# Kernel optimization log

Hardware: AMD Instinct MI355X
Metric: run time of the kernel (lower is better)

Reference implementation:

```python
import jax, jax.numpy as jnp
import numpy as np

B = 2048
N_USERS = 100000
N_ITEMS = 50000
N = N_USERS + N_ITEMS
EMB = 64
NNZ = 100000


def setup_inputs() -> dict:
    key = jax.random.key(0)
    k1, k2, k3, k4 = jax.random.split(key, 4)
    u_id = jax.random.randint(k1, (B,), 0, N_USERS, dtype=jnp.int64 if jax.config.jax_enable_x64 else jnp.int32)
    pos_i_id = jax.random.randint(k2, (B,), 0, N, dtype=u_id.dtype)
    train_mask = jax.random.randint(k3, (2, NNZ), 0, B, dtype=u_id.dtype)
    all_embed = jax.random.normal(k4, (N, EMB), dtype=jnp.float32)
    return {"u_id": u_id, "pos_i_id": pos_i_id, "train_mask": train_mask, "all_embed": all_embed}


def reference(u_id, pos_i_id, train_mask, all_embed):
    # policy_type == 'uij': scores = (u_e + pos_e) @ all_e^T  -> [B, N]
    u_e = all_embed[u_id]
    pos_e = all_embed[pos_i_id]
    scores = jnp.einsum("bd,nd->bn", u_e + pos_e, all_embed)
    # Note: the original computes a sparse train-mask tensor (sp_mask) but never
    # uses it; only the zero->-inf masking below affects the output.
    logits = jnp.where(scores == 0.0, -jnp.inf, scores)
    probs = jax.nn.softmax(logits, axis=1)  # [B, N]
    # Categorical sampling per row (fixed key for reproducibility)
    samples = jax.random.categorical(jax.random.key(42), logits, axis=1)  # [B]
    selected_neg_prob = jnp.take_along_axis(probs, samples[:, None], axis=1)[:, 0]
    return samples, selected_neg_prob
```

## Files before the change

### kernel.cpp

```cpp
#include <hip/hip_runtime.h>
#include <stdint.h>

#define B_ROWS   2048
#define N_COLS   150000
#define NSTRIPS  128
#define CHUNK    128
#define NCHUNK   1172
#define ROWG     16

#define NEG_HUGE (-3.0e38f)
#define G_SPAN_HARD  20.6f
#define G_MAX_MARGIN 15.944f
#define EPS_B        2.0e-4f
#define G_FILTER_SLACK 1e-5f

#define WS_MPART 0
#define WS_ZPART (B_ROWS * NSTRIPS)
#define WS_CMAX  (2 * B_ROWS * NSTRIPS)
#define WS_M     (WS_CMAX + B_ROWS * NCHUNK)
#define WS_Z     (WS_M + B_ROWS)
#define WS_VLB   (WS_Z + B_ROWS)
#define WS_CSTAR (WS_VLB + B_ROWS)
#define WS_BEST  (WS_CSTAR + B_ROWS)
#define WS_ENORM (WS_BEST + 2 * B_ROWS)
#define WS_QNORM (WS_ENORM + 2048)
#define WS_EHI   (WS_QNORM + B_ROWS)
#define WS_ELO   (WS_EHI + NCHUNK * 4096)
#define WS_END   (WS_ELO + NCHUNK * 4096)

typedef __attribute__((ext_vector_type(8))) unsigned short ushort8;
typedef __attribute__((ext_vector_type(8))) short short8;
typedef __attribute__((ext_vector_type(4))) float f32x4;

__device__ __forceinline__ uint32_t rotl32(uint32_t x, int r) {
  return (x << r) | (x >> (32 - r));
}

__device__ __forceinline__ void threefry2x32_k42(uint32_t& x0, uint32_t& x1) {
  const uint32_t ks0 = 0u;
  const uint32_t ks1 = 42u;
  const uint32_t ks2 = 0x1BD11BDAu ^ 0u ^ 42u;
  x0 += ks0; x1 += ks1;
#define TF_R(r) { x0 += x1; x1 = rotl32(x1, (r)); x1 ^= x0; }
  TF_R(13) TF_R(15) TF_R(26) TF_R(6)
  x0 += ks1; x1 += ks2 + 1u;
  TF_R(17) TF_R(29) TF_R(16) TF_R(24)
  x0 += ks2; x1 += ks0 + 2u;
  TF_R(13) TF_R(15) TF_R(26) TF_R(6)
  x0 += ks0; x1 += ks1 + 3u;
  TF_R(17) TF_R(29) TF_R(16) TF_R(24)
  x0 += ks1; x1 += ks2 + 4u;
  TF_R(13) TF_R(15) TF_R(26) TF_R(6)
  x0 += ks2; x1 += ks0 + 5u;
#undef TF_R
}

__device__ __forceinline__ float gumbel_from_bits(uint32_t bits) {
  const uint32_t mant = bits >> 9;
  const float f = __uint_as_float(mant | 0x3f800000u) - 1.0f;
  const float l1 = mant ? log1pf(f - 1.0f) : -87.33654475055311f;
  return -__logf(-l1);
}

__device__ __forceinline__ float gumbel_at(uint32_t flat_idx) {
  uint32_t x0 = 0u, x1 = flat_idx;
  threefry2x32_k42(x0, x1);
  return gumbel_from_bits(x0 ^ x1);
}

__device__ __forceinline__ unsigned long long pack_vn(float v, int n) {
  uint32_t u = __float_as_uint(v);
  u ^= ((uint32_t)((int32_t)u >> 31)) | 0x80000000u;
  return ((unsigned long long)u << 32) | (uint32_t)(0xFFFFFFFFu - (uint32_t)n);
}

__device__ __forceinline__ float unpack_v(unsigned long long p) {
  uint32_t u = (uint32_t)(p >> 32);
  u = (u & 0x80000000u) ? (u ^ 0x80000000u) : ~u;
  return __uint_as_float(u);
}

__device__ __forceinline__ int unpack_n(unsigned long long p) {
  return (int)(0xFFFFFFFFu - (uint32_t)(p & 0xFFFFFFFFull));
}

__device__ __forceinline__ unsigned long long umax64(unsigned long long a,
                                                     unsigned long long b) {
  return a > b ? a : b;
}

__device__ __forceinline__ float dot_q_e(const float4* q4, const float4* e4) {
  float s = 0.0f;
#pragma unroll
  for (int k4 = 0; k4 < 16; ++k4) {
    const float4 e = e4[k4];
    const float4 q = q4[k4];
    s = fmaf(q.x, e.x, s);
    s = fmaf(q.y, e.y, s);
    s = fmaf(q.z, e.z, s);
    s = fmaf(q.w, e.w, s);
  }
  return s;
}

__device__ __forceinline__ unsigned short f32_to_bf16_rne(float f) {
  const uint32_t u = __float_as_uint(f);
  return (unsigned short)((u + 0x7fffu + ((u >> 16) & 1u)) >> 16);
}
__device__ __forceinline__ float bf16_to_f32(unsigned short h) {
  return __uint_as_float(((uint32_t)h) << 16);
}

__global__ __launch_bounds__(256) void advnet_enorm(const float* __restrict__ emb,
                                                    float* __restrict__ ws) {
  const int c = blockIdx.x;
  const int t = threadIdx.x;
  const int lane = t & 63;
  const int row = t >> 1;
  const int n = c * CHUNK + row;
  float ss = 0.0f;
  if (n < N_COLS) {
    const float4* p = (const float4*)emb + (size_t)n * 16 + (t & 1) * 8;
#pragma unroll
    for (int i = 0; i < 8; ++i) {
      const float4 v = p[i];
      ss = fmaf(v.x, v.x, ss); ss = fmaf(v.y, v.y, ss);
      ss = fmaf(v.z, v.z, ss); ss = fmaf(v.w, v.w, ss);
    }
  }
  ss += __shfl_xor(ss, 1, 64);
  float mx = ss;
  for (int off = 2; off < 64; off <<= 1) mx = fmaxf(mx, __shfl_xor(mx, off, 64));
  __shared__ float sm[4];
  if (lane == 0) sm[t >> 6] = mx;
  __syncthreads();
  if (t == 0)
    ws[WS_ENORM + c] =
        sqrtf(fmaxf(fmaxf(sm[0], sm[1]), fmaxf(sm[2], sm[3]))) * 1.00002f;
}

__global__ __launch_bounds__(256) void advnet_ebuild(const float* __restrict__ emb,
                                                     float* __restrict__ ws) {
  const int c = blockIdx.x;
  const int t = threadIdx.x;
  char* hi_b = (char*)(ws + WS_EHI) + (size_t)c * 16384;
  char* lo_b = (char*)(ws + WS_ELO) + (size_t)c * 16384;
#pragma unroll
  for (int k = 0; k < 4; ++k) {
    const int j = t + 256 * k;
    const int row = j >> 3, kq = j & 7;
    const int n = c * CHUNK + row;
    ushort8 hi = (ushort8)0, lo = (ushort8)0;
    if (n < N_COLS) {
      const float4* ep = (const float4*)emb + (size_t)n * 16 + kq * 2;
      const float4 a0 = ep[0], a1 = ep[1];
      const float e[8] = {a0.x, a0.y, a0.z, a0.w, a1.x, a1.y, a1.z, a1.w};
#pragma unroll
      for (int j8 = 0; j8 < 8; ++j8) {
        const unsigned short h = f32_to_bf16_rne(e[j8]);
        hi[j8] = h;
        lo[j8] = f32_to_bf16_rne(e[j8] - bf16_to_f32(h));
      }
    }
    const int gz = kq ^ (row & 7);
    *(ushort8*)(hi_b + (size_t)(row * 8 + gz) * 16) = hi;
    *(ushort8*)(lo_b + (size_t)(row * 8 + gz) * 16) = lo;
  }
}

__device__ __forceinline__ void stage_tbl(const char* tb_hi, const char* tb_lo,
                                          unsigned short* eh, unsigned short* el,
                                          int c, int wave, int lane) {
  const size_t cb = (size_t)c * 16384 + (size_t)(wave * 1024 + lane * 16);
  const int wo = wave * 1024;
#pragma unroll
  for (int i = 0; i < 4; ++i) {
    const int off = i * 4096;
    __builtin_amdgcn_global_load_lds(
        (const __attribute__((address_space(1))) void*)(tb_hi + cb + off),
        (__attribute__((address_space(3))) void*)((char*)eh + wo + off), 16, 0, 0);
    __builtin_amdgcn_global_load_lds(
        (const __attribute__((address_space(1))) void*)(tb_lo + cb + off),
        (__attribute__((address_space(3))) void*)((char*)el + wo + off), 16, 0, 0);
  }
}

__device__ __forceinline__ void stage_conv(const float* __restrict__ emb,
                                           unsigned short* eh, unsigned short* el,
                                           int c, int tid) {
  const int n0 = c * CHUNK;
#pragma unroll
  for (int k = 0; k < 4; ++k) {
    const int p = tid + 256 * k;
    const int row = p >> 3, kq = p & 7;
    const int n = n0 + row;
    ushort8 hi = (ushort8)0, lo = (ushort8)0;
    if (n < N_COLS) {
      const float4* ep = (const float4*)emb + (size_t)n * 16 + kq * 2;
      const float4 a0 = ep[0], a1 = ep[1];
      const float e[8] = {a0.x, a0.y, a0.z, a0.w, a1.x, a1.y, a1.z, a1.w};
#pragma unroll
      for (int j = 0; j < 8; ++j) {
        const unsigned short h = f32_to_bf16_rne(e[j]);
        hi[j] = h;
        lo[j] = f32_to_bf16_rne(e[j] - bf16_to_f32(h));
      }
    }
    const int off = row * 64 + ((kq * 8) ^ ((row & 7) << 3));
    *(ushort8*)&eh[off] = hi;
    *(ushort8*)&el[off] = lo;
  }
}

template <bool TBL>
__global__ __launch_bounds__(256, 2) void advnet_gemm(
    const int* __restrict__ u_id, const int* __restrict__ pos_id,
    const float* __restrict__ emb, float* __restrict__ ws) {
  __shared__ unsigned short eh0[8192], el0[8192], eh1[8192], el1[8192];

  const int tid = threadIdx.x;
  const int bid = blockIdx.x;
  const int rg = bid / NSTRIPS;
  const int strip = bid - rg * NSTRIPS;
  const int wave = tid >> 6;
  const int lane = tid & 63;
  const int lc = lane & 15;
  const int lg = lane >> 4;

#pragma unroll
  for (int k = 0; k < 4; ++k) {
    const int p = tid + 256 * k;
    const int row = p >> 3, kq = p & 7;
    const int b = rg * 128 + row;
    const float4* ua = (const float4*)emb + (size_t)u_id[b] * 16 + kq * 2;
    const float4* pa = (const float4*)emb + (size_t)pos_id[b] * 16 + kq * 2;
    const float4 a0 = ua[0], a1 = ua[1], c0 = pa[0], c1 = pa[1];
    const float q[8] = {a0.x + c0.x, a0.y + c0.y, a0.z + c0.z, a0.w + c0.w,
                        a1.x + c1.x, a1.y + c1.y, a1.z + c1.z, a1.w + c1.w};
    ushort8 hi, lo;
#pragma unroll
    for (int j = 0; j < 8; ++j) {
      const unsigned short h = f32_to_bf16_rne(q[j]);
      hi[j] = h;
      lo[j] = f32_to_bf16_rne(q[j] - bf16_to_f32(h));
    }
    const int off = row * 64 + ((kq * 8) ^ ((row & 7) << 3));
    *(ushort8*)&eh0[off] = hi;
    *(ushort8*)&el0[off] = lo;
  }
  __syncthreads();

  short8 qh_r[2][2], ql_r[2][2];
#pragma unroll
  for (int kh = 0; kh < 2; ++kh)
#pragma unroll
    for (int rt = 0; rt < 2; ++rt) {
      const int r = wave * 32 + rt * 16 + lc;
      const int off = r * 64 + (((kh * 4 + lg) * 8) ^ ((r & 7) << 3));
      qh_r[kh][rt] = *(const short8*)&eh0[off];
      ql_r[kh][rt] = *(const short8*)&el0[off];
    }
  __syncthreads();

  float m[8], Z[8];
#pragma unroll
  for (int s = 0; s < 8; ++s) { m[s] = NEG_HUGE; Z[s] = 0.0f; }

  const char* tb_hi = (const char*)(ws + WS_EHI);
  const char* tb_lo = (const char*)(ws + WS_ELO);

  if (TBL) stage_tbl(tb_hi, tb_lo, eh0, el0, strip, wave, lane);
  else     stage_conv(emb, eh0, el0, strip, tid);
  __syncthreads();

  int cur = 0;
  for (int c = strip; c < NCHUNK; c += NSTRIPS) {
    unsigned short* EH  = cur ? eh1 : eh0;
    unsigned short* EL  = cur ? el1 : el0;
    unsigned short* EHn = cur ? eh0 : eh1;
    unsigned short* ELn = cur ? el0 : el1;
    if (c + NSTRIPS < NCHUNK) {
      if (TBL) stage_tbl(tb_hi, tb_lo, EHn, ELn, c + NSTRIPS, wave, lane);
      else     stage_conv(emb, EHn, ELn, c + NSTRIPS, tid);
    }

    f32x4 acc[2][8];
#pragma unroll
    for (int rt = 0; rt < 2; ++rt)
#pragma unroll
      for (int ct = 0; ct < 8; ++ct) acc[rt][ct] = (f32x4){0.f, 0.f, 0.f, 0.f};

#pragma unroll
    for (int kh = 0; kh < 2; ++kh) {
#pragma unroll
      for (int ct = 0; ct < 8; ++ct) {
        const int col = ct * 16 + lc;
        const int off = col * 64 + (((kh * 4 + lg) * 8) ^ ((col & 7) << 3));
        const short8 ehf = *(const short8*)&EH[off];
        const short8 elf = *(const short8*)&EL[off];
#pragma unroll
        for (int rt = 0; rt < 2; ++rt) {
          acc[rt][ct] = __builtin_amdgcn_mfma_f32_16x16x32_bf16(qh_r[kh][rt], ehf, acc[rt][ct], 0, 0, 0);
          acc[rt][ct] = __builtin_amdgcn_mfma_f32_16x16x32_bf16(qh_r[kh][rt], elf, acc[rt][ct], 0, 0, 0);
          acc[rt][ct] = __builtin_amdgcn_mfma_f32_16x16x32_bf16(ql_r[kh][rt], ehf, acc[rt][ct], 0, 0, 0);
        }
      }
    }

#pragma unroll
    for (int rt = 0; rt < 2; ++rt) {
#pragma unroll
      for (int j = 0; j < 4; ++j) {
        const int s = rt * 4 + j;
        float sp[8];
        float cm = NEG_HUGE;
#pragma unroll
        for (int ct = 0; ct < 8; ++ct) {
          const float v = acc[rt][ct][j];
          sp[ct] = (v != 0.0f) ? v : NEG_HUGE;
          cm = fmaxf(cm, sp[ct]);
        }
        const float nm = fmaxf(m[s], cm);
        float za = 0.0f;
#pragma unroll
        for (int ct = 0; ct < 8; ++ct) za += __expf(sp[ct] - nm);
        Z[s] = Z[s] * __expf(m[s] - nm) + za;
        m[s] = nm;
        float cr = cm;
        cr = fmaxf(cr, __shfl_xor(cr, 1, 64));
        cr = fmaxf(cr, __shfl_xor(cr, 2, 64));
        cr = fmaxf(cr, __shfl_xor(cr, 4, 64));
        cr = fmaxf(cr, __shfl_xor(cr, 8, 64));
        if (lc == 0) {
          const int row = rg * 128 + wave * 32 + rt * 16 + lg * 4 + j;
          ws[WS_CMAX + (size_t)row * NCHUNK + c] = cr;
        }
      }
    }
    __syncthreads();
    cur ^= 1;
  }

#pragma unroll
  for (int rt = 0; rt < 2; ++rt) {
#pragma unroll
    for (int j = 0; j < 4; ++j) {
      const int s = rt * 4 + j;
      float mi = m[s], Zi = Z[s];
      for (int off = 1; off < 16; off <<= 1) {
        const float om = __shfl_xor(mi, off, 64);
        const float oZ = __shfl_xor(Zi, off, 64);
        const float nm = fmaxf(mi, om);
        Zi = Zi * __expf(mi - nm) + oZ * __expf(om - nm);
        mi = nm;
      }
      if (lc == 0) {
        const int row = rg * 128 + wave * 32 + rt * 16 + lg * 4 + j;
        ws[WS_MPART + (size_t)row * NSTRIPS + strip] = mi;
        ws[WS_ZPART + (size_t)row * NSTRIPS + strip] = Zi;
      }
    }
  }
}

__global__ __launch_bounds__(128) void advnet_rowstat(
    const int* __restrict__ u_id, const int* __restrict__ pos_id,
    const float* __restrict__ emb, float* __restrict__ ws) {
  const int r = blockIdx.x;
  const int t = threadIdx.x;

  __shared__ float sA[2], sB[2];
  __shared__ unsigned long long sP[2];
  __shared__ float qrow[64];

  const size_t idx = (size_t)r * NSTRIPS + t;
  const float ms = ws[WS_MPART + idx];
  const float zs = ws[WS_ZPART + idx];
  float M = ms;
  for (int off = 1; off < 64; off <<= 1) M = fmaxf(M, __shfl_xor(M, off, 64));
  if ((t & 63) == 0) sA[t >> 6] = M;
  __syncthreads();
  M = fmaxf(sA[0], sA[1]);
  float z = zs * __expf(ms - M);
  for (int off = 1; off < 64; off <<= 1) z += __shfl_xor(z, off, 64);
  if ((t & 63) == 0) sB[t >> 6] = z;
  __syncthreads();
  const float Z = sB[0] + sB[1];

  unsigned long long cp = 0ull;
  for (int c = t; c < NCHUNK; c += 128)
    cp = umax64(cp, pack_vn(ws[WS_CMAX + (size_t)r * NCHUNK + c], c));
  for (int off = 1; off < 64; off <<= 1)
    cp = umax64(cp, __shfl_xor(cp, off, 64));
  if ((t & 63) == 0) sP[t >> 6] = cp;
  __syncthreads();
  cp = umax64(sP[0], sP[1]);
  const int cstar = unpack_n(cp);

  if (t < 16) {
    const float4 a = ((const float4*)emb)[(size_t)u_id[r] * 16 + t];
    const float4 c = ((const float4*)emb)[(size_t)pos_id[r] * 16 + t];
    ((float4*)qrow)[t] = make_float4(a.x + c.x, a.y + c.y, a.z + c.z, a.w + c.w);
  }
  __syncthreads();

  {
    const float qv = qrow[t & 63];
    float ss = qv * qv;
    for (int off = 1; off < 64; off <<= 1) ss += __shfl_xor(ss, off, 64);
    if (t == 0) ws[WS_QNORM + r] = sqrtf(ss) * 1.00002f;
  }

  unsigned long long bp = 0ull;
  const int n = cstar * CHUNK + t;
  if (n < N_COLS) {
    const float s = dot_q_e((const float4*)qrow, (const float4*)emb + (size_t)n * 16);
    if (s != 0.0f && s >= M - G_SPAN_HARD) {
      const uint32_t L = (uint32_t)r * (uint32_t)N_COLS + (uint32_t)n;
      bp = pack_vn(gumbel_at(L) + s, n);
    }
  }
  for (int off = 1; off < 64; off <<= 1)
    bp = umax64(bp, __shfl_xor(bp, off, 64));
  if ((t & 63) == 0) sP[t >> 6] = bp;
  __syncthreads();
  if (t == 0) {
    const unsigned long long best = umax64(sP[0], sP[1]);
    ((unsigned long long*)(ws + WS_BEST))[r] = best;
    ws[WS_VLB + r] = unpack_v(best);
    ws[WS_M + r] = M;
    ws[WS_Z + r] = Z;
    ((int*)ws)[WS_CSTAR + r] = cstar;
  }
}

#define SVCAP 2048
__global__ __launch_bounds__(256) void advnet_pick(
    const int* __restrict__ u_id, const int* __restrict__ pos_id,
    const float* __restrict__ emb, float* __restrict__ ws) {
  const int r = blockIdx.x >> 1;
  const int par = blockIdx.x & 1;
  const int t = threadIdx.x;

  __shared__ float qrow[64];
  __shared__ unsigned short cq[600];
  __shared__ float cqg[600];
  __shared__ unsigned int svpk[SVCAP];
  __shared__ float svg[SVCAP];
  __shared__ int cqn, svn;
  __shared__ unsigned long long sred[4];

  if (t == 0) { cqn = 0; svn = 0; }
  if (t < 16) {
    const float4 a = ((const float4*)emb)[(size_t)u_id[r] * 16 + t];
    const float4 c = ((const float4*)emb)[(size_t)pos_id[r] * 16 + t];
    ((float4*)qrow)[t] = make_float4(a.x + c.x, a.y + c.y, a.z + c.z, a.w + c.w);
  }
  const float vlb = ws[WS_VLB + r];
  const float bq = ws[WS_QNORM + r] * EPS_B;
  const int cstar = ((const int*)ws)[WS_CSTAR + r];
  __syncthreads();

  for (int c = par + 2 * t; c < NCHUNK; c += 512) {
    if (c == cstar) continue;
    const float cm = ws[WS_CMAX + (size_t)r * NCHUNK + c];
    const float gth = vlb - cm - bq * ws[WS_ENORM + c];
    if (gth < G_MAX_MARGIN) {
      const int k = atomicAdd(&cqn, 1);
      cq[k] = (unsigned short)c;
      cqg[k] = gth;
    }
  }
  __syncthreads();
  const int nq = cqn;
  const float4* qr4 = (const float4*)qrow;

  unsigned long long bp = 0ull;

  for (int base = 0; base < nq; base += 8) {
    if (svn > SVCAP - 1024) {
      __syncthreads();
      const int cnt = svn;
      for (int k = t; k < cnt; k += 256) {
        const int n = (int)svpk[k];
        const float s = dot_q_e(qr4, (const float4*)emb + (size_t)n * 16);
        if (s != 0.0f) bp = umax64(bp, pack_vn(svg[k] + s, n));
      }
      __syncthreads();
      if (t == 0) svn = 0;
      __syncthreads();
    }
#pragma unroll
    for (int u = 0; u < 4; ++u) {
      const int idx = t + 256 * u;
      const int slot = base + (idx >> 7);
      if (slot < nq) {
        const int n = (int)cq[slot] * CHUNK + (idx & 127);
        if (n < N_COLS) {
          const float g = gumbel_at((uint32_t)r * (uint32_t)N_COLS + (uint32_t)n);
          if (g > cqg[slot] - G_FILTER_SLACK) {
            const int k = atomicAdd(&svn, 1);
            if (k < SVCAP) { svpk[k] = (unsigned)n; svg[k] = g; }
          }
        }
      }
    }
    __syncthreads();
  }

  {
    const int cnt = svn < SVCAP ? svn : SVCAP;
    for (int k = t; k < cnt; k += 256) {
      const int n = (int)svpk[k];
      const float s = dot_q_e(qr4, (const float4*)emb + (size_t)n * 16);
      if (s != 0.0f) bp = umax64(bp, pack_vn(svg[k] + s, n));
    }
  }

  for (int off = 1; off < 64; off <<= 1)
    bp = umax64(bp, __shfl_xor(bp, off, 64));
  if ((t & 63) == 0) sred[t >> 6] = bp;
  __syncthreads();
  if (t == 0) {
    const unsigned long long b =
        umax64(umax64(sred[0], sred[1]), umax64(sred[2], sred[3]));
    if (b) atomicMax((unsigned long long*)(ws + WS_BEST) + r, b);
  }
}

__global__ __launch_bounds__(64) void advnet_final(
    const int* __restrict__ u_id, const int* __restrict__ pos_id,
    const float* __restrict__ emb, const float* __restrict__ ws,
    float* __restrict__ out) {
  const int r = blockIdx.x * 64 + threadIdx.x;
  if (r >= B_ROWS) return;
  const unsigned long long w = ((const unsigned long long*)(ws + WS_BEST))[r];
  const int n = unpack_n(w);
  const float4* qa = (const float4*)emb + (size_t)u_id[r] * 16;
  const float4* qb = (const float4*)emb + (size_t)pos_id[r] * 16;
  const float4* e4 = (const float4*)emb + (size_t)n * 16;
  float s = 0.0f;
#pragma unroll
  for (int k4 = 0; k4 < 16; ++k4) {
    const float4 a = qa[k4], b = qb[k4], e = e4[k4];
    float4 q;
    q.x = a.x + b.x; q.y = a.y + b.y; q.z = a.z + b.z; q.w = a.w + b.w;
    s = fmaf(q.x, e.x, s);
    s = fmaf(q.y, e.y, s);
    s = fmaf(q.z, e.z, s);
    s = fmaf(q.w, e.w, s);
  }
  out[r] = (float)n;
  out[B_ROWS + r] = __expf(s - ws[WS_M + r]) / ws[WS_Z + r];
}

extern "C" void kernel_launch(void* const* d_in, const int* in_sizes, int n_in,
                              void* d_out, int out_size, void* d_ws, size_t ws_size,
                              hipStream_t stream) {
  const int* u_id = (const int*)d_in[0];
  const int* pos_id = (const int*)d_in[1];
  const float* emb = (const float*)d_in[3];
  float* ws = (float*)d_ws;
  float* out = (float*)d_out;

  const size_t need = (size_t)WS_END * 4;
  const bool tbl = ws_size >= need;

  advnet_enorm<<<dim3(NCHUNK), dim3(256), 0, stream>>>(emb, ws);
  if (tbl) {
    advnet_ebuild<<<dim3(NCHUNK), dim3(256), 0, stream>>>(emb, ws);
    advnet_gemm<true><<<dim3(ROWG * NSTRIPS), dim3(256), 0, stream>>>(
        u_id, pos_id, emb, ws);
  } else {
    advnet_gemm<false><<<dim3(ROWG * NSTRIPS), dim3(256), 0, stream>>>(
        u_id, pos_id, emb, ws);
  }
  advnet_rowstat<<<dim3(B_ROWS), dim3(128), 0, stream>>>(u_id, pos_id, emb, ws);
  advnet_pick<<<dim3(B_ROWS * 2), dim3(256), 0, stream>>>(u_id, pos_id, emb, ws);
  advnet_final<<<dim3(B_ROWS / 64), dim3(64), 0, stream>>>(u_id, pos_id, emb, ws, out);
}
```

Before: 306.9 us.

## Fold enorm into ebuild, single-buffer GEMM LDS, use exp2 with pre-scaled queries

The row-norm computation moves into the ebuild kernel, so one launch and one full read of the embedding table go away when the workspace is large enough. The GEMM drops LDS double buffering for a single buffer, which raises the occupancy hint from 2 to 5 blocks per CU but serialises loads and compute inside each block. Queries are pre-scaled by log2(e) so the online softmax can use the native exp2. The explicit zero-score masking in the max/sum loop is removed, and the sampling filter slack is loosened to absorb the extra rounding.

```diff
diff --git a/kernel.cpp b/kernel.cpp
--- a/kernel.cpp
+++ b/kernel.cpp
@@ -12,7 +12,16 @@
 #define G_SPAN_HARD  20.6f
 #define G_MAX_MARGIN 15.944f
 #define EPS_B        2.0e-4f
-#define G_FILTER_SLACK 1e-5f
+#define G_FILTER_SLACK 3e-5f
+
+#define LOG2E_F 1.44269504088896340736f
+#define LN2_F   0.69314718055994530942f
+
+#if __has_builtin(__builtin_amdgcn_exp2f)
+#define EXP2F(x) __builtin_amdgcn_exp2f(x)
+#else
+#define EXP2F(x) exp2f(x)
+#endif
 
 #define WS_MPART 0
 #define WS_ZPART (B_ROWS * NSTRIPS)
@@ -145,12 +154,14 @@
   const int t = threadIdx.x;
   char* hi_b = (char*)(ws + WS_EHI) + (size_t)c * 16384;
   char* lo_b = (char*)(ws + WS_ELO) + (size_t)c * 16384;
+  float mx = 0.0f;
 #pragma unroll
   for (int k = 0; k < 4; ++k) {
     const int j = t + 256 * k;
     const int row = j >> 3, kq = j & 7;
     const int n = c * CHUNK + row;
     ushort8 hi = (ushort8)0, lo = (ushort8)0;
+    float ss = 0.0f;
     if (n < N_COLS) {
       const float4* ep = (const float4*)emb + (size_t)n * 16 + kq * 2;
       const float4 a0 = ep[0], a1 = ep[1];
@@ -160,12 +171,24 @@
         const unsigned short h = f32_to_bf16_rne(e[j8]);
         hi[j8] = h;
         lo[j8] = f32_to_bf16_rne(e[j8] - bf16_to_f32(h));
+        ss = fmaf(e[j8], e[j8], ss);
       }
     }
     const int gz = kq ^ (row & 7);
     *(ushort8*)(hi_b + (size_t)(row * 8 + gz) * 16) = hi;
     *(ushort8*)(lo_b + (size_t)(row * 8 + gz) * 16) = lo;
-  }
+    ss += __shfl_xor(ss, 1, 64);
+    ss += __shfl_xor(ss, 2, 64);
+    ss += __shfl_xor(ss, 4, 64);
+    mx = fmaxf(mx, ss);
+  }
+  for (int off = 8; off < 64; off <<= 1) mx = fmaxf(mx, __shfl_xor(mx, off, 64));
+  __shared__ float sm[4];
+  if ((t & 63) == 0) sm[t >> 6] = mx;
+  __syncthreads();
+  if (t == 0)
+    ws[WS_ENORM + c] =
+        sqrtf(fmaxf(fmaxf(sm[0], sm[1]), fmaxf(sm[2], sm[3]))) * 1.00002f;
 }
 
 __device__ __forceinline__ void stage_tbl(const char* tb_hi, const char* tb_lo,
@@ -213,10 +236,10 @@
 }
 
 template <bool TBL>
-__global__ __launch_bounds__(256, 2) void advnet_gemm(
+__global__ __launch_bounds__(256, 5) void advnet_gemm(
     const int* __restrict__ u_id, const int* __restrict__ pos_id,
     const float* __restrict__ emb, float* __restrict__ ws) {
-  __shared__ unsigned short eh0[8192], el0[8192], eh1[8192], el1[8192];
+  __shared__ unsigned short eh_s[8192], el_s[8192];
 
   const int tid = threadIdx.x;
   const int bid = blockIdx.x;
@@ -235,8 +258,10 @@
     const float4* ua = (const float4*)emb + (size_t)u_id[b] * 16 + kq * 2;
     const float4* pa = (const float4*)emb + (size_t)pos_id[b] * 16 + kq * 2;
     const float4 a0 = ua[0], a1 = ua[1], c0 = pa[0], c1 = pa[1];
-    const float q[8] = {a0.x + c0.x, a0.y + c0.y, a0.z + c0.z, a0.w + c0.w,
-                        a1.x + c1.x, a1.y + c1.y, a1.z + c1.z, a1.w + c1.w};
+    const float q[8] = {(a0.x + c0.x) * LOG2E_F, (a0.y + c0.y) * LOG2E_F,
+                        (a0.z + c0.z) * LOG2E_F, (a0.w + c0.w) * LOG2E_F,
+                        (a1.x + c1.x) * LOG2E_F, (a1.y + c1.y) * LOG2E_F,
+                        (a1.z + c1.z) * LOG2E_F, (a1.w + c1.w) * LOG2E_F};
     ushort8 hi, lo;
 #pragma unroll
     for (int j = 0; j < 8; ++j) {
@@ -245,8 +270,8 @@
       lo[j] = f32_to_bf16_rne(q[j] - bf16_to_f32(h));
     }
     const int off = row * 64 + ((kq * 8) ^ ((row & 7) << 3));
-    *(ushort8*)&eh0[off] = hi;
-    *(ushort8*)&el0[off] = lo;
+    *(ushort8*)&eh_s[off] = hi;
+    *(ushort8*)&el_s[off] = lo;
   }
   __syncthreads();
 
@@ -257,8 +282,8 @@
     for (int rt = 0; rt < 2; ++rt) {
       const int r = wave * 32 + rt * 16 + lc;
       const int off = r * 64 + (((kh * 4 + lg) * 8) ^ ((r & 7) << 3));
-      qh_r[kh][rt] = *(const short8*)&eh0[off];
-      ql_r[kh][rt] = *(const short8*)&el0[off];
+      qh_r[kh][rt] = *(const short8*)&eh_s[off];
+      ql_r[kh][rt] = *(const short8*)&el_s[off];
     }
   __syncthreads();
 
@@ -269,20 +294,10 @@
   const char* tb_hi = (const char*)(ws + WS_EHI);
   const char* tb_lo = (const char*)(ws + WS_ELO);
 
-  if (TBL) stage_tbl(tb_hi, tb_lo, eh0, el0, strip, wave, lane);
-  else     stage_conv(emb, eh0, el0, strip, tid);
-  __syncthreads();
-
-  int cur = 0;
   for (int c = strip; c < NCHUNK; c += NSTRIPS) {
-    unsigned short* EH  = cur ? eh1 : eh0;
-    unsigned short* EL  = cur ? el1 : el0;
-    unsigned short* EHn = cur ? eh0 : eh1;
-    unsigned short* ELn = cur ? el0 : el1;
-    if (c + NSTRIPS < NCHUNK) {
-      if (TBL) stage_tbl(tb_hi, tb_lo, EHn, ELn, c + NSTRIPS, wave, lane);
-      else     stage_conv(emb, EHn, ELn, c + NSTRIPS, tid);
-    }
+    if (TBL) stage_tbl(tb_hi, tb_lo, eh_s, el_s, c, wave, lane);
+    else     stage_conv(emb, eh_s, el_s, c, tid);
+    __syncthreads();
 
     f32x4 acc[2][8];
 #pragma unroll
@@ -296,8 +311,8 @@
       for (int ct = 0; ct < 8; ++ct) {
         const int col = ct * 16 + lc;
         const int off = col * 64 + (((kh * 4 + lg) * 8) ^ ((col & 7) << 3));
-        const short8 ehf = *(const short8*)&EH[off];
-        const short8 elf = *(const short8*)&EL[off];
+        const short8 ehf = *(const short8*)&eh_s[off];
+        const short8 elf = *(const short8*)&el_s[off];
 #pragma unroll
         for (int rt = 0; rt < 2; ++rt) {
           acc[rt][ct] = __builtin_amdgcn_mfma_f32_16x16x32_bf16(qh_r[kh][rt], ehf, acc[rt][ct], 0, 0, 0);
@@ -312,19 +327,14 @@
 #pragma unroll
       for (int j = 0; j < 4; ++j) {
         const int s = rt * 4 + j;
-        float sp[8];
-        float cm = NEG_HUGE;
-#pragma unroll
-        for (int ct = 0; ct < 8; ++ct) {
-          const float v = acc[rt][ct][j];
-          sp[ct] = (v != 0.0f) ? v : NEG_HUGE;
-          cm = fmaxf(cm, sp[ct]);
-        }
+        float cm = acc[rt][0][j];
+#pragma unroll
+        for (int ct = 1; ct < 8; ++ct) cm = fmaxf(cm, acc[rt][ct][j]);
         const float nm = fmaxf(m[s], cm);
         float za = 0.0f;
 #pragma unroll
-        for (int ct = 0; ct < 8; ++ct) za += __expf(sp[ct] - nm);
-        Z[s] = Z[s] * __expf(m[s] - nm) + za;
+        for (int ct = 0; ct < 8; ++ct) za += EXP2F(acc[rt][ct][j] - nm);
+        Z[s] = Z[s] * EXP2F(m[s] - nm) + za;
         m[s] = nm;
         float cr = cm;
         cr = fmaxf(cr, __shfl_xor(cr, 1, 64));
@@ -338,7 +348,6 @@
       }
     }
     __syncthreads();
-    cur ^= 1;
   }
 
 #pragma unroll
@@ -351,7 +360,7 @@
         const float om = __shfl_xor(mi, off, 64);
         const float oZ = __shfl_xor(Zi, off, 64);
         const float nm = fmaxf(mi, om);
-        Zi = Zi * __expf(mi - nm) + oZ * __expf(om - nm);
+        Zi = Zi * EXP2F(mi - nm) + oZ * EXP2F(om - nm);
         mi = nm;
       }
       if (lc == 0) {
@@ -376,16 +385,17 @@
   const size_t idx = (size_t)r * NSTRIPS + t;
   const float ms = ws[WS_MPART + idx];
   const float zs = ws[WS_ZPART + idx];
-  float M = ms;
-  for (int off = 1; off < 64; off <<= 1) M = fmaxf(M, __shfl_xor(M, off, 64));
-  if ((t & 63) == 0) sA[t >> 6] = M;
-  __syncthreads();
-  M = fmaxf(sA[0], sA[1]);
-  float z = zs * __expf(ms - M);
+  float Ms = ms;
+  for (int off = 1; off < 64; off <<= 1) Ms = fmaxf(Ms, __shfl_xor(Ms, off, 64));
+  if ((t & 63) == 0) sA[t >> 6] = Ms;
+  __syncthreads();
+  Ms = fmaxf(sA[0], sA[1]);
+  float z = zs * EXP2F(ms - Ms);
   for (int off = 1; off < 64; off <<= 1) z += __shfl_xor(z, off, 64);
   if ((t & 63) == 0) sB[t >> 6] = z;
   __syncthreads();
   const float Z = sB[0] + sB[1];
+  const float M_nat = Ms * LN2_F;
 
   unsigned long long cp = 0ull;
   for (int c = t; c < NCHUNK; c += 128)
@@ -415,7 +425,7 @@
   const int n = cstar * CHUNK + t;
   if (n < N_COLS) {
     const float s = dot_q_e((const float4*)qrow, (const float4*)emb + (size_t)n * 16);
-    if (s != 0.0f && s >= M - G_SPAN_HARD) {
+    if (s != 0.0f && s >= M_nat - G_SPAN_HARD) {
       const uint32_t L = (uint32_t)r * (uint32_t)N_COLS + (uint32_t)n;
       bp = pack_vn(gumbel_at(L) + s, n);
     }
@@ -428,7 +438,7 @@
     const unsigned long long best = umax64(sP[0], sP[1]);
     ((unsigned long long*)(ws + WS_BEST))[r] = best;
     ws[WS_VLB + r] = unpack_v(best);
-    ws[WS_M + r] = M;
+    ws[WS_M + r] = M_nat;
     ws[WS_Z + r] = Z;
     ((int*)ws)[WS_CSTAR + r] = cstar;
   }
@@ -464,7 +474,7 @@
   for (int c = par + 2 * t; c < NCHUNK; c += 512) {
     if (c == cstar) continue;
     const float cm = ws[WS_CMAX + (size_t)r * NCHUNK + c];
-    const float gth = vlb - cm - bq * ws[WS_ENORM + c];
+    const float gth = vlb - fmaf(cm, LN2_F, bq * ws[WS_ENORM + c]);
     if (gth < G_MAX_MARGIN) {
       const int k = atomicAdd(&cqn, 1);
       cq[k] = (unsigned short)c;
@@ -566,12 +576,12 @@
   const size_t need = (size_t)WS_END * 4;
   const bool tbl = ws_size >= need;
 
-  advnet_enorm<<<dim3(NCHUNK), dim3(256), 0, stream>>>(emb, ws);
   if (tbl) {
     advnet_ebuild<<<dim3(NCHUNK), dim3(256), 0, stream>>>(emb, ws);
     advnet_gemm<true><<<dim3(ROWG * NSTRIPS), dim3(256), 0, stream>>>(
         u_id, pos_id, emb, ws);
   } else {
+    advnet_enorm<<<dim3(NCHUNK), dim3(256), 0, stream>>>(emb, ws);
     advnet_gemm<false><<<dim3(ROWG * NSTRIPS), dim3(256), 0, stream>>>(
         u_id, pos_id, emb, ws);
   }
```

Measured after the change: 480.1 us. 1.56x slower.
